# Performance work log

Measured on AMD Instinct MI355X. Metric: run time of the kernel, lower is better.

## Reference

```python
import jax, jax.numpy as jnp
import numpy as np

B, V, D = 8, 2048, 3
CL1_F, CL1_K = 64, 6
CL2_F, CL2_K = 128, 5
F1, F2 = 512, 256


def _uniform(k, shape, fin, fout):
    s = np.sqrt(2.0 / (fin + fout)).astype(np.float32)
    return jax.random.uniform(k, shape, jnp.float32, -s, s)


def setup_inputs() -> dict:
    key = jax.random.key(0)
    ks = jax.random.split(key, 8)
    x = jax.random.normal(ks[0], (B, D, V), jnp.float32)
    # dense stand-in for the scaled graph Laplacian; scaled so spectral radius < 1
    L = jax.random.normal(ks[1], (B, V, V), jnp.float32) * (0.5 / np.sqrt(V))
    L = 0.5 * (L + L.transpose(0, 2, 1))  # symmetric like a real Laplacian
    return {
        "x": x,
        "L": L,
        "cl1_w": _uniform(ks[2], (CL1_F, D * CL1_K), CL1_K, CL1_F),
        "cl1_b": jnp.zeros((CL1_F,), jnp.float32),
        "cl2_w": _uniform(ks[3], (CL2_F, CL2_K * CL1_F), CL2_K * CL1_F, CL2_F),
        "cl2_b": jnp.zeros((CL2_F,), jnp.float32),
        "fc1_w": _uniform(ks[4], (F1, CL2_F), CL2_F, F1),
        "fc1_b": jnp.zeros((F1,), jnp.float32),
        "fc2_w": _uniform(ks[5], (F2, F1), F1, F2),
        "fc2_b": jnp.zeros((F2,), jnp.float32),
    }


def _cheby_conv(x, L, W, b, K):
    # x: [B, V, Fin], L: [B, V, V] -> [B, V, Fout]
    x0 = x
    xs = [x0]
    if K > 1:
        x1 = jnp.einsum('bvu,buf->bvf', L, x0)
        xs.append(x1)
    for _ in range(2, K):
        x2 = 2.0 * jnp.einsum('bvu,buf->bvf', L, x1) - x0
        xs.append(x2)
        x0, x1 = x1, x2
    # torch ordering: feature index = fin * K + k  -> stack K on last axis
    xk = jnp.stack(xs, axis=-1)                 # [B, V, Fin, K]
    xk = xk.reshape(xk.shape[0], xk.shape[1], -1)  # [B, V, Fin*K]
    return xk @ W.T + b


def reference(x, L, cl1_w, cl1_b, cl2_w, cl2_b, fc1_w, fc1_b, fc2_w, fc2_b):
    xp = x.transpose(0, 2, 1)                    # [B, V, D]
    y = jax.nn.relu(_cheby_conv(xp, L, cl1_w, cl1_b, CL1_K))
    y = jax.nn.relu(_cheby_conv(y, L, cl2_w, cl2_b, CL2_K))
    y = jax.nn.relu(y @ fc1_w.T + fc1_b)
    y = jax.nn.relu(y @ fc2_w.T + fc2_b)
    return y                                     # [B, V, F2]
```

## Files before the change

### kernel.cpp

```cpp
#include <hip/hip_runtime.h>

#define B_ 8
#define V_ 2048
#define D_ 3
#define M_ (B_*V_)

typedef __attribute__((ext_vector_type(8))) short short8;
typedef __attribute__((ext_vector_type(4))) float f32x4;

__device__ inline void async_copy16(const void* g, void* lds) {
  __builtin_amdgcn_global_load_lds(
      (const __attribute__((address_space(1))) unsigned int*)g,
      (__attribute__((address_space(3))) unsigned int*)lds, 16, 0, 0);
}

__device__ inline void split_bf16(float v, short& hi, short& lo) {
  unsigned u  = __float_as_uint(v);
  unsigned hb = u & 0xFFFF0000u;
  float d = v - __uint_as_float(hb);
  hi = (short)(hb >> 16);
  lo = (short)(__float_as_uint(d) >> 16);
}

__global__ __launch_bounds__(256) void k_zero(float4* __restrict__ p, int n4) {
  int i = blockIdx.x * 256 + threadIdx.x;
  if (i < n4) p[i] = float4{0.f, 0.f, 0.f, 0.f};
}

__global__ __launch_bounds__(256) void k_split_pad(const float* __restrict__ src,
    short* __restrict__ dh, short* __restrict__ dl, int N, int K, int Kpad) {
  int idx = blockIdx.x * 256 + threadIdx.x;
  if (idx >= N * Kpad) return;
  int n = idx / Kpad, k = idx - n * Kpad;
  float v = (k < K) ? src[(size_t)n*K + k] : 0.f;
  short hi, lo; split_bf16(v, hi, lo);
  dh[idx] = hi; dl[idx] = lo;
}

__global__ __launch_bounds__(256) void k_transpose(const float* __restrict__ x,
    float* __restrict__ x0, short* __restrict__ XKh, short* __restrict__ XKl) {
  int i = blockIdx.x * 256 + threadIdx.x;
  if (i >= B_*V_*D_) return;
  int f = i % D_;
  int v = (i / D_) % V_;
  int b = i / (D_*V_);
  float val = x[((size_t)b*D_ + f)*V_ + v];
  x0[i] = val;
  short hi, lo; split_bf16(val, hi, lo);
  size_t o = ((size_t)b*V_ + v)*64 + f*6;
  XKh[o] = hi; XKl[o] = lo;
}

__global__ __launch_bounds__(256) void k_cheby1(const float* __restrict__ L,
    const float* __restrict__ xc, const float* __restrict__ xp,
    float* __restrict__ xn, short* __restrict__ XKh, short* __restrict__ XKl,
    float alpha, float beta, int kidx) {
  __shared__ float sx[3][V_];
  int b  = blockIdx.x >> 6;
  int r0 = (blockIdx.x & 63) * 32;
  const float* xcb = xc + (size_t)b*V_*D_;
  for (int i = threadIdx.x; i < V_*D_; i += 256) {
    int u = i / 3, f = i - u*3;
    sx[f][u] = xcb[i];
  }
  __syncthreads();
  int w = threadIdx.x >> 6, lane = threadIdx.x & 63;
  const float4* X0 = (const float4*)sx[0];
  const float4* X1 = (const float4*)sx[1];
  const float4* X2 = (const float4*)sx[2];
  for (int pass = 0; pass < 4; pass++) {
    int rA = r0 + pass*8 + w*2;
    int rB = rA + 1;
    const float4* LA = (const float4*)(L + ((size_t)b*V_ + rA)*V_);
    const float4* LB = (const float4*)(L + ((size_t)b*V_ + rB)*V_);
    float a0=0.f,a1=0.f,a2=0.f,b0=0.f,b1=0.f,b2=0.f;
    #pragma unroll
    for (int it = 0; it < 8; it++) {
      int u4 = it*64 + lane;
      float4 la = LA[u4], lb = LB[u4];
      float4 x0 = X0[u4], x1 = X1[u4], x2 = X2[u4];
      a0 = fmaf(la.x,x0.x,fmaf(la.y,x0.y,fmaf(la.z,x0.z,fmaf(la.w,x0.w,a0))));
      a1 = fmaf(la.x,x1.x,fmaf(la.y,x1.y,fmaf(la.z,x1.z,fmaf(la.w,x1.w,a1))));
      a2 = fmaf(la.x,x2.x,fmaf(la.y,x2.y,fmaf(la.z,x2.z,fmaf(la.w,x2.w,a2))));
      b0 = fmaf(lb.x,x0.x,fmaf(lb.y,x0.y,fmaf(lb.z,x0.z,fmaf(lb.w,x0.w,b0))));
      b1 = fmaf(lb.x,x1.x,fmaf(lb.y,x1.y,fmaf(lb.z,x1.z,fmaf(lb.w,x1.w,b1))));
      b2 = fmaf(lb.x,x2.x,fmaf(lb.y,x2.y,fmaf(lb.z,x2.z,fmaf(lb.w,x2.w,b2))));
    }
    #pragma unroll
    for (int off = 32; off > 0; off >>= 1) {
      a0 += __shfl_down(a0, off); a1 += __shfl_down(a1, off);
      a2 += __shfl_down(a2, off); b0 += __shfl_down(b0, off);
      b1 += __shfl_down(b1, off); b2 += __shfl_down(b2, off);
    }
    if (lane == 0) {
      float vA[3] = {alpha*a0, alpha*a1, alpha*a2};
      float vB[3] = {alpha*b0, alpha*b1, alpha*b2};
      size_t baseA = ((size_t)b*V_ + rA)*3;
      size_t baseB = ((size_t)b*V_ + rB)*3;
      if (beta != 0.f) {
        #pragma unroll
        for (int f = 0; f < 3; f++) {
          vA[f] -= beta * xp[baseA + f];
          vB[f] -= beta * xp[baseB + f];
        }
      }
      #pragma unroll
      for (int f = 0; f < 3; f++) {
        xn[baseA + f] = vA[f];
        xn[baseB + f] = vB[f];
        short hi, lo;
        split_bf16(vA[f], hi, lo);
        size_t oA = ((size_t)b*V_ + rA)*64 + f*6 + kidx;
        XKh[oA] = hi; XKl[oA] = lo;
        split_bf16(vB[f], hi, lo);
        size_t oB = ((size_t)b*V_ + rB)*64 + f*6 + kidx;
        XKh[oB] = hi; XKl[oB] = lo;
      }
    }
  }
}

__global__ __launch_bounds__(256) void k_split_t(const float* __restrict__ Z,
    short* __restrict__ Th, short* __restrict__ Tl) {
  __shared__ float t[64][65];
  int b  = blockIdx.x >> 5;
  int r0 = (blockIdx.x & 31) * 64;
  const float* Zb = Z + ((size_t)b*V_ + r0)*64;
  #pragma unroll 4
  for (int i = 0; i < 16; i++) {
    int idx = i*256 + threadIdx.x;
    int r = idx >> 6, n = idx & 63;
    t[r][n] = Zb[(size_t)r*64 + n];
  }
  __syncthreads();
  #pragma unroll 4
  for (int i = 0; i < 16; i++) {
    int idx = i*256 + threadIdx.x;
    int n = idx >> 6, r = idx & 63;
    short hi, lo; split_bf16(t[r][n], hi, lo);
    size_t o = ((size_t)b*64 + n)*V_ + r0 + r;
    Th[o] = hi; Tl[o] = lo;
  }
}

__global__ __launch_bounds__(256) void k_cheby2_mfma(const float* __restrict__ L,
    const short* __restrict__ Zth, const short* __restrict__ Ztl,
    const float* __restrict__ Zp,
    float* __restrict__ Zn, short* __restrict__ ZKh, short* __restrict__ ZKl,
    short* __restrict__ Znth, short* __restrict__ Zntl,
    float alpha, float beta, int kidx) {
  __shared__ float sA[32*64];
  __shared__ short sBh[64*64];
  __shared__ short sBl[64*64];

  int b  = blockIdx.x >> 6;
  int r0 = (blockIdx.x & 63) * 32;
  const float* Lb   = L   + (size_t)b*V_*V_;
  const short* Zthb = Zth + (size_t)b*64*V_;
  const short* Ztlb = Ztl + (size_t)b*64*V_;

  int tid  = threadIdx.x;
  int w    = tid >> 6;
  int lane = tid & 63;
  int lm   = lane & 15;
  int quad = lane >> 4;
  int h     = (w & 1) * 16;
  int cbase = (w >> 1) * 32;

  const f32x4*  sAv  = (const f32x4*)sA;
  const short8* sBhv = (const short8*)sBh;
  const short8* sBlv = (const short8*)sBl;

  f32x4 acc0 = {0.f,0.f,0.f,0.f};
  f32x4 acc1 = {0.f,0.f,0.f,0.f};

  for (int s = 0; s < V_/64; s++) {
    int k0 = s * 64;
    if (s) __syncthreads();
    #pragma unroll
    for (int t = 0; t < 2; t++) {
      int f = t*256 + tid;
      int r = f >> 4, cc = f & 15;
      int c = cc ^ (r & 15);
      async_copy16(Lb + (size_t)(r0 + r)*V_ + k0 + c*4, &sA[f*4]);
    }
    #pragma unroll
    for (int t = 0; t < 2; t++) {
      int f = t*256 + tid;
      int n = f >> 3, cc = f & 7;
      int c = cc ^ (n & 7);
      async_copy16(Zthb + (size_t)n*V_ + k0 + c*8, &sBh[f*8]);
      async_copy16(Ztlb + (size_t)n*V_ + k0 + c*8, &sBl[f*8]);
    }
    __syncthreads();

    #pragma unroll
    for (int ks = 0; ks < 2; ks++) {
      int koff = ks * 32;
      int r = h + lm;
      int c0 = (koff >> 2) + 2*quad;
      f32x4 a0 = sAv[r*16 + (c0 ^ (r & 15))];
      f32x4 a1 = sAv[r*16 + ((c0 + 1) ^ (r & 15))];
      float av[8] = {a0.x, a0.y, a0.z, a0.w, a1.x, a1.y, a1.z, a1.w};
      short8 ah, al;
      #pragma unroll
      for (int j = 0; j < 8; j++) {
        short hi, lo; split_bf16(av[j], hi, lo);
        ah[j] = hi; al[j] = lo;
      }
      int cb = (koff >> 3) + quad;
      {
        int n = cbase + lm;
        short8 bh = sBhv[n*8 + (cb ^ (n & 7))];
        short8 bl = sBlv[n*8 + (cb ^ (n & 7))];
        acc0 = __builtin_amdgcn_mfma_f32_16x16x32_bf16(ah, bh, acc0, 0, 0, 0);
        acc0 = __builtin_amdgcn_mfma_f32_16x16x32_bf16(ah, bl, acc0, 0, 0, 0);
        acc0 = __builtin_amdgcn_mfma_f32_16x16x32_bf16(al, bh, acc0, 0, 0, 0);
      }
      {
        int n = cbase + 16 + lm;
        short8 bh = sBhv[n*8 + (cb ^ (n & 7))];
        short8 bl = sBlv[n*8 + (cb ^ (n & 7))];
        acc1 = __builtin_amdgcn_mfma_f32_16x16x32_bf16(ah, bh, acc1, 0, 0, 0);
        acc1 = __builtin_amdgcn_mfma_f32_16x16x32_bf16(ah, bl, acc1, 0, 0, 0);
        acc1 = __builtin_amdgcn_mfma_f32_16x16x32_bf16(al, bh, acc1, 0, 0, 0);
      }
    }
  }

  #pragma unroll
  for (int ct = 0; ct < 2; ct++) {
    f32x4 a = ct ? acc1 : acc0;
    int n = cbase + ct*16 + lm;
    #pragma unroll
    for (int i = 0; i < 4; i++) {
      int r = r0 + h + quad*4 + i;
      size_t rowb = (size_t)b*V_ + r;
      float v = alpha * a[i];
      if (beta != 0.f) v -= beta * Zp[rowb*64 + n];
      Zn[rowb*64 + n] = v;
      short hi, lo; split_bf16(v, hi, lo);
      size_t ok = rowb*320 + (size_t)n*5 + kidx;
      ZKh[ok] = hi; ZKl[ok] = lo;
      size_t o = ((size_t)b*64 + n)*V_ + r;
      Znth[o] = hi; Zntl[o] = lo;
    }
  }
}

__global__ __launch_bounds__(256) void k_gemm_bf16(
    const short* __restrict__ Ah, const short* __restrict__ Al,
    const short* __restrict__ Wh, const short* __restrict__ Wl,
    const float* __restrict__ bias, int N, int K,
    float* __restrict__ Cf, short* __restrict__ Ch, short* __restrict__ Cl,
    short* __restrict__ Ph, short* __restrict__ Pl,
    int packMul, int packStride) {
  __shared__ short sAh[64*64], sAl[64*64], sWh[64*64], sWl[64*64];
  int bm = blockIdx.x & 255;
  int bn = blockIdx.x >> 8;
  int row0 = bm * 64, col0 = bn * 64;
  int tid = threadIdx.x, w = tid >> 6, lane = tid & 63;
  int lm = lane & 15, quad = lane >> 4;
  int wm = (w & 1) * 32, wn = (w >> 1) * 32;

  const short8* vAh = (const short8*)sAh;
  const short8* vAl = (const short8*)sAl;
  const short8* vWh = (const short8*)sWh;
  const short8* vWl = (const short8*)sWl;

  f32x4 acc[2][2] = {{{0.f,0.f,0.f,0.f},{0.f,0.f,0.f,0.f}},
                     {{0.f,0.f,0.f,0.f},{0.f,0.f,0.f,0.f}}};

  for (int k0 = 0; k0 < K; k0 += 64) {
    if (k0) __syncthreads();
    #pragma unroll
    for (int t = 0; t < 2; t++) {
      int f = t*256 + tid;
      int r = f >> 3, p = f & 7;
      int c = p ^ (r & 7);
      size_t goA = (size_t)(row0 + r)*K + k0 + c*8;
      size_t goW = (size_t)(col0 + r)*K + k0 + c*8;
      async_copy16(Ah + goA, &sAh[f*8]);
      async_copy16(Al + goA, &sAl[f*8]);
      async_copy16(Wh + goW, &sWh[f*8]);
      async_copy16(Wl + goW, &sWl[f*8]);
    }
    __syncthreads();

    #pragma unroll
    for (int ks = 0; ks < 2; ks++) {
      int kc = ks*4 + quad;
      short8 a_h[2], a_l[2], b_h[2], b_l[2];
      #pragma unroll
      for (int i = 0; i < 2; i++) {
        int m = wm + i*16 + lm;
        a_h[i] = vAh[m*8 + (kc ^ (m & 7))];
        a_l[i] = vAl[m*8 + (kc ^ (m & 7))];
      }
      #pragma unroll
      for (int j = 0; j < 2; j++) {
        int n = wn + j*16 + lm;
        b_h[j] = vWh[n*8 + (kc ^ (n & 7))];
        b_l[j] = vWl[n*8 + (kc ^ (n & 7))];
      }
      #pragma unroll
      for (int i = 0; i < 2; i++)
        #pragma unroll
        for (int j = 0; j < 2; j++) {
          acc[i][j] = __builtin_amdgcn_mfma_f32_16x16x32_bf16(a_h[i], b_h[j], acc[i][j], 0, 0, 0);
          acc[i][j] = __builtin_amdgcn_mfma_f32_16x16x32_bf16(a_h[i], b_l[j], acc[i][j], 0, 0, 0);
          acc[i][j] = __builtin_amdgcn_mfma_f32_16x16x32_bf16(a_l[i], b_h[j], acc[i][j], 0, 0, 0);
        }
    }
  }

  #pragma unroll
  for (int i = 0; i < 2; i++)
    #pragma unroll
    for (int j = 0; j < 2; j++) {
      int col = col0 + wn + j*16 + lm;
      float bj = bias[col];
      #pragma unroll
      for (int g = 0; g < 4; g++) {
        int row = row0 + wm + i*16 + quad*4 + g;
        float v = acc[i][j][g] + bj;
        v = v > 0.f ? v : 0.f;
        if (Cf) Cf[(size_t)row*N + col] = v;
        if (Ch) {
          short hi, lo; split_bf16(v, hi, lo);
          Ch[(size_t)row*N + col] = hi;
          Cl[(size_t)row*N + col] = lo;
        }
        if (Ph) {
          short hi, lo; split_bf16(v, hi, lo);
          size_t o = (size_t)row*packStride + (size_t)col*packMul;
          Ph[o] = hi; Pl[o] = lo;
        }
      }
    }
}

extern "C" void kernel_launch(void* const* d_in, const int* in_sizes, int n_in,
                              void* d_out, int out_size, void* d_ws, size_t ws_size,
                              hipStream_t stream) {
  const float* x   = (const float*)d_in[0];
  const float* L   = (const float*)d_in[1];
  const float* w1  = (const float*)d_in[2];
  const float* b1  = (const float*)d_in[3];
  const float* w2  = (const float*)d_in[4];
  const float* b2  = (const float*)d_in[5];
  const float* fw1 = (const float*)d_in[6];
  const float* fb1 = (const float*)d_in[7];
  const float* fw2 = (const float*)d_in[8];
  const float* fb2 = (const float*)d_in[9];
  float* out = (float*)d_out;

  float* p  = (float*)d_ws;
  float* xa = p;  p += (size_t)B_*V_*D_;
  float* xb = p;  p += (size_t)B_*V_*D_;
  float* xc = p;  p += (size_t)B_*V_*D_;
  float* y1 = p;  p += (size_t)M_*64;
  float* zb = p;  p += (size_t)M_*64;
  float* zc = p;  p += (size_t)M_*64;
  short* sp = (short*)p;
  short* ZKh = sp;  sp += (size_t)M_*320;
  short* ZKl = sp;  sp += (size_t)M_*320;
  short* y2h = sp;  sp += (size_t)M_*128;
  short* y2l = sp;  sp += (size_t)M_*128;
  short* h1h = sp;  sp += (size_t)M_*512;
  short* h1l = sp;  sp += (size_t)M_*512;
  short* ZtAh = sp; sp += (size_t)M_*64;
  short* ZtAl = sp; sp += (size_t)M_*64;
  short* ZtBh = sp; sp += (size_t)M_*64;
  short* ZtBl = sp; sp += (size_t)M_*64;
  short* w1h = sp;  sp += 64*64;
  short* w1l = sp;  sp += 64*64;
  short* w2h = sp;  sp += 128*320;
  short* w2l = sp;  sp += 128*320;
  short* fw1h = sp; sp += 512*128;
  short* fw1l = sp; sp += 512*128;
  short* fw2h = sp; sp += 256*512;
  short* fw2l = sp; sp += 256*512;
  short* XKh = h1h;
  short* XKl = h1h + (size_t)M_*64;

  dim3 blk(256);

  k_zero<<<1024, blk, 0, stream>>>((float4*)XKh, (M_*128) / 8);

  k_split_pad<<<(64*64+255)/256,   blk, 0, stream>>>(w1,  w1h,  w1l,  64, 18, 64);
  k_split_pad<<<(128*320+255)/256, blk, 0, stream>>>(w2,  w2h,  w2l,  128, 320, 320);
  k_split_pad<<<(512*128+255)/256, blk, 0, stream>>>(fw1, fw1h, fw1l, 512, 128, 128);
  k_split_pad<<<(256*512+255)/256, blk, 0, stream>>>(fw2, fw2h, fw2l, 256, 512, 512);

  k_transpose<<<(B_*V_*D_ + 255)/256, blk, 0, stream>>>(x, xa, XKh, XKl);

  k_cheby1<<<512, blk, 0, stream>>>(L, xa, xa, xb, XKh, XKl, 1.f, 0.f, 1);
  k_cheby1<<<512, blk, 0, stream>>>(L, xb, xa, xc, XKh, XKl, 2.f, 1.f, 2);
  k_cheby1<<<512, blk, 0, stream>>>(L, xc, xb, xa, XKh, XKl, 2.f, 1.f, 3);
  k_cheby1<<<512, blk, 0, stream>>>(L, xa, xc, xb, XKh, XKl, 2.f, 1.f, 4);
  k_cheby1<<<512, blk, 0, stream>>>(L, xb, xa, xc, XKh, XKl, 2.f, 1.f, 5);

  k_gemm_bf16<<<256, blk, 0, stream>>>(XKh, XKl, w1h, w1l, b1, 64, 64,
                                       y1, nullptr, nullptr, ZKh, ZKl, 5, 320);

  k_split_t<<<256, blk, 0, stream>>>(y1, ZtAh, ZtAl);

  k_cheby2_mfma<<<512, blk, 0, stream>>>(L, ZtAh, ZtAl, y1, zb, ZKh, ZKl,
                                         ZtBh, ZtBl, 1.f, 0.f, 1);
  k_cheby2_mfma<<<512, blk, 0, stream>>>(L, ZtBh, ZtBl, y1, zc, ZKh, ZKl,
                                         ZtAh, ZtAl, 2.f, 1.f, 2);
  k_cheby2_mfma<<<512, blk, 0, stream>>>(L, ZtAh, ZtAl, zb, y1, ZKh, ZKl,
                                         ZtBh, ZtBl, 2.f, 1.f, 3);
  k_cheby2_mfma<<<512, blk, 0, stream>>>(L, ZtBh, ZtBl, zc, zb, ZKh, ZKl,
                                         ZtAh, ZtAl, 2.f, 1.f, 4);

  k_gemm_bf16<<<512, blk, 0, stream>>>(ZKh, ZKl, w2h, w2l, b2, 128, 320,
                                       nullptr, y2h, y2l, nullptr, nullptr, 0, 0);
  k_gemm_bf16<<<2048, blk, 0, stream>>>(y2h, y2l, fw1h, fw1l, fb1, 512, 128,
                                        nullptr, h1h, h1l, nullptr, nullptr, 0, 0);
  k_gemm_bf16<<<1024, blk, 0, stream>>>(h1h, h1l, fw2h, fw2l, fb2, 256, 512,
                                        out, nullptr, nullptr, nullptr, nullptr, 0, 0);
}
```

Measured before the change: 594.7 us.

## Merge stage launches into cooperative persistent kernels with grid syncs

Replaces many small launches with a few: a combined prep kernel (zeroing, transpose, weight splitting), cooperative kernels that run all Chebyshev steps of each layer with grid.sync between steps, and a cooperative kernel chaining the three dense GEMMs. The layer-1 GEMM epilogue now also writes the transposed bf16 split, which removes the separate transpose kernel. The aim is to cut launch gaps and inter-kernel idle time. In exchange it relies on 512 blocks being co-resident and adds grid-wide barrier cost, and the FC GEMMs with 2048 or 1024 tiles now loop over a fixed 512-block grid.

```diff
diff --git a/kernel.cpp b/kernel.cpp
--- a/kernel.cpp
+++ b/kernel.cpp
@@ -1,4 +1,7 @@
 #include <hip/hip_runtime.h>
+#include <hip/hip_cooperative_groups.h>
+
+namespace cg = cooperative_groups;
 
 #define B_ 8
 #define V_ 2048
@@ -22,243 +25,139 @@
   lo = (short)(__float_as_uint(d) >> 16);
 }
 
-__global__ __launch_bounds__(256) void k_zero(float4* __restrict__ p, int n4) {
+__global__ __launch_bounds__(256) void k_prep(
+    const float* __restrict__ x,
+    const float* __restrict__ w1, const float* __restrict__ w2,
+    const float* __restrict__ fw1, const float* __restrict__ fw2,
+    float* __restrict__ xa,
+    short* __restrict__ XKh, short* __restrict__ XKl,
+    short* __restrict__ w1h, short* __restrict__ w1l,
+    short* __restrict__ w2h, short* __restrict__ w2l,
+    short* __restrict__ fw1h, short* __restrict__ fw1l,
+    short* __restrict__ fw2h, short* __restrict__ fw2l) {
   int i = blockIdx.x * 256 + threadIdx.x;
-  if (i < n4) p[i] = float4{0.f, 0.f, 0.f, 0.f};
-}
-
-__global__ __launch_bounds__(256) void k_split_pad(const float* __restrict__ src,
-    short* __restrict__ dh, short* __restrict__ dl, int N, int K, int Kpad) {
-  int idx = blockIdx.x * 256 + threadIdx.x;
-  if (idx >= N * Kpad) return;
-  int n = idx / Kpad, k = idx - n * Kpad;
-  float v = (k < K) ? src[(size_t)n*K + k] : 0.f;
-  short hi, lo; split_bf16(v, hi, lo);
-  dh[idx] = hi; dl[idx] = lo;
-}
-
-__global__ __launch_bounds__(256) void k_transpose(const float* __restrict__ x,
-    float* __restrict__ x0, short* __restrict__ XKh, short* __restrict__ XKl) {
-  int i = blockIdx.x * 256 + threadIdx.x;
-  if (i >= B_*V_*D_) return;
-  int f = i % D_;
-  int v = (i / D_) % V_;
-  int b = i / (D_*V_);
-  float val = x[((size_t)b*D_ + f)*V_ + v];
-  x0[i] = val;
-  short hi, lo; split_bf16(val, hi, lo);
-  size_t o = ((size_t)b*V_ + v)*64 + f*6;
-  XKh[o] = hi; XKl[o] = lo;
-}
-
-__global__ __launch_bounds__(256) void k_cheby1(const float* __restrict__ L,
-    const float* __restrict__ xc, const float* __restrict__ xp,
-    float* __restrict__ xn, short* __restrict__ XKh, short* __restrict__ XKl,
-    float alpha, float beta, int kidx) {
+  short hi, lo;
+  if (i < M_*64) {
+    int r = i >> 6, s = i & 63;
+    float val = 0.f;
+    if (s == 0 || s == 6 || s == 12) {
+      int f = s / 6;
+      int b = r >> 11, v = r & (V_-1);
+      val = x[((size_t)b*D_ + f)*V_ + v];
+      xa[(size_t)r*3 + f] = val;
+    }
+    split_bf16(val, hi, lo);
+    XKh[i] = hi; XKl[i] = lo;
+    return;
+  }
+  i -= M_*64;
+  if (i < 4096) {
+    int n = i >> 6, k = i & 63;
+    float v = (k < 18) ? w1[n*18 + k] : 0.f;
+    split_bf16(v, hi, lo); w1h[i] = hi; w1l[i] = lo; return;
+  }
+  i -= 4096;
+  if (i < 40960) { split_bf16(w2[i],  hi, lo); w2h[i]=hi;  w2l[i]=lo;  return; }
+  i -= 40960;
+  if (i < 65536) { split_bf16(fw1[i], hi, lo); fw1h[i]=hi; fw1l[i]=lo; return; }
+  i -= 65536;
+  if (i < 131072){ split_bf16(fw2[i], hi, lo); fw2h[i]=hi; fw2l[i]=lo; return; }
+}
+
+__global__ __launch_bounds__(256, 2) void k_cheby1_all(
+    const float* __restrict__ L, float* __restrict__ xa,
+    float* __restrict__ xb, float* __restrict__ xc,
+    short* __restrict__ XKh, short* __restrict__ XKl) {
+  cg::grid_group grid = cg::this_grid();
   __shared__ float sx[3][V_];
+
+  const float* srcs[5]  = {xa, xb, xc, xa, xb};
+  const float* prevs[5] = {xa, xa, xb, xc, xa};
+  float*       dsts[5]  = {xb, xc, xa, xb, xc};
+
   int b  = blockIdx.x >> 6;
   int r0 = (blockIdx.x & 63) * 32;
-  const float* xcb = xc + (size_t)b*V_*D_;
-  for (int i = threadIdx.x; i < V_*D_; i += 256) {
-    int u = i / 3, f = i - u*3;
-    sx[f][u] = xcb[i];
-  }
-  __syncthreads();
   int w = threadIdx.x >> 6, lane = threadIdx.x & 63;
-  const float4* X0 = (const float4*)sx[0];
-  const float4* X1 = (const float4*)sx[1];
-  const float4* X2 = (const float4*)sx[2];
-  for (int pass = 0; pass < 4; pass++) {
-    int rA = r0 + pass*8 + w*2;
-    int rB = rA + 1;
-    const float4* LA = (const float4*)(L + ((size_t)b*V_ + rA)*V_);
-    const float4* LB = (const float4*)(L + ((size_t)b*V_ + rB)*V_);
-    float a0=0.f,a1=0.f,a2=0.f,b0=0.f,b1=0.f,b2=0.f;
-    #pragma unroll
-    for (int it = 0; it < 8; it++) {
-      int u4 = it*64 + lane;
-      float4 la = LA[u4], lb = LB[u4];
-      float4 x0 = X0[u4], x1 = X1[u4], x2 = X2[u4];
-      a0 = fmaf(la.x,x0.x,fmaf(la.y,x0.y,fmaf(la.z,x0.z,fmaf(la.w,x0.w,a0))));
-      a1 = fmaf(la.x,x1.x,fmaf(la.y,x1.y,fmaf(la.z,x1.z,fmaf(la.w,x1.w,a1))));
-      a2 = fmaf(la.x,x2.x,fmaf(la.y,x2.y,fmaf(la.z,x2.z,fmaf(la.w,x2.w,a2))));
-      b0 = fmaf(lb.x,x0.x,fmaf(lb.y,x0.y,fmaf(lb.z,x0.z,fmaf(lb.w,x0.w,b0))));
-      b1 = fmaf(lb.x,x1.x,fmaf(lb.y,x1.y,fmaf(lb.z,x1.z,fmaf(lb.w,x1.w,b1))));
-      b2 = fmaf(lb.x,x2.x,fmaf(lb.y,x2.y,fmaf(lb.z,x2.z,fmaf(lb.w,x2.w,b2))));
-    }
-    #pragma unroll
-    for (int off = 32; off > 0; off >>= 1) {
-      a0 += __shfl_down(a0, off); a1 += __shfl_down(a1, off);
-      a2 += __shfl_down(a2, off); b0 += __shfl_down(b0, off);
-      b1 += __shfl_down(b1, off); b2 += __shfl_down(b2, off);
-    }
-    if (lane == 0) {
-      float vA[3] = {alpha*a0, alpha*a1, alpha*a2};
-      float vB[3] = {alpha*b0, alpha*b1, alpha*b2};
-      size_t baseA = ((size_t)b*V_ + rA)*3;
-      size_t baseB = ((size_t)b*V_ + rB)*3;
-      if (beta != 0.f) {
+
+  for (int step = 0; step < 5; step++) {
+    float alpha = (step == 0) ? 1.f : 2.f;
+    bool  haveP = (step != 0);
+    const float* xcb = srcs[step] + (size_t)b*V_*D_;
+    const float* xp  = prevs[step];
+    float* xn = dsts[step];
+    int kidx = step + 1;
+
+    for (int i = threadIdx.x; i < V_*D_; i += 256) {
+      int u = i / 3, f = i - u*3;
+      sx[f][u] = xcb[i];
+    }
+    __syncthreads();
+
+    const float4* X0 = (const float4*)sx[0];
+    const float4* X1 = (const float4*)sx[1];
+    const float4* X2 = (const float4*)sx[2];
+    for (int pass = 0; pass < 4; pass++) {
+      int rA = r0 + pass*8 + w*2;
+      int rB = rA + 1;
+      const float4* LA = (const float4*)(L + ((size_t)b*V_ + rA)*V_);
+      const float4* LB = (const float4*)(L + ((size_t)b*V_ + rB)*V_);
+      float a0=0.f,a1=0.f,a2=0.f,b0=0.f,b1=0.f,b2=0.f;
+      #pragma unroll
+      for (int it = 0; it < 8; it++) {
+        int u4 = it*64 + lane;
+        float4 la = LA[u4], lb = LB[u4];
+        float4 x0 = X0[u4], x1 = X1[u4], x2 = X2[u4];
+        a0 = fmaf(la.x,x0.x,fmaf(la.y,x0.y,fmaf(la.z,x0.z,fmaf(la.w,x0.w,a0))));
+        a1 = fmaf(la.x,x1.x,fmaf(la.y,x1.y,fmaf(la.z,x1.z,fmaf(la.w,x1.w,a1))));
+        a2 = fmaf(la.x,x2.x,fmaf(la.y,x2.y,fmaf(la.z,x2.z,fmaf(la.w,x2.w,a2))));
+        b0 = fmaf(lb.x,x0.x,fmaf(lb.y,x0.y,fmaf(lb.z,x0.z,fmaf(lb.w,x0.w,b0))));
+        b1 = fmaf(lb.x,x1.x,fmaf(lb.y,x1.y,fmaf(lb.z,x1.z,fmaf(lb.w,x1.w,b1))));
+        b2 = fmaf(lb.x,x2.x,fmaf(lb.y,x2.y,fmaf(lb.z,x2.z,fmaf(lb.w,x2.w,b2))));
+      }
+      #pragma unroll
+      for (int off = 32; off > 0; off >>= 1) {
+        a0 += __shfl_down(a0, off); a1 += __shfl_down(a1, off);
+        a2 += __shfl_down(a2, off); b0 += __shfl_down(b0, off);
+        b1 += __shfl_down(b1, off); b2 += __shfl_down(b2, off);
+      }
+      if (lane == 0) {
+        float vA[3] = {alpha*a0, alpha*a1, alpha*a2};
+        float vB[3] = {alpha*b0, alpha*b1, alpha*b2};
+        size_t baseA = ((size_t)b*V_ + rA)*3;
+        size_t baseB = ((size_t)b*V_ + rB)*3;
+        if (haveP) {
+          #pragma unroll
+          for (int f = 0; f < 3; f++) {
+            vA[f] -= xp[baseA + f];
+            vB[f] -= xp[baseB + f];
+          }
+        }
         #pragma unroll
         for (int f = 0; f < 3; f++) {
-          vA[f] -= beta * xp[baseA + f];
-          vB[f] -= beta * xp[baseB + f];
-        }
-      }
-      #pragma unroll
-      for (int f = 0; f < 3; f++) {
-        xn[baseA + f] = vA[f];
-        xn[baseB + f] = vB[f];
-        short hi, lo;
-        split_bf16(vA[f], hi, lo);
-        size_t oA = ((size_t)b*V_ + rA)*64 + f*6 + kidx;
-        XKh[oA] = hi; XKl[oA] = lo;
-        split_bf16(vB[f], hi, lo);
-        size_t oB = ((size_t)b*V_ + rB)*64 + f*6 + kidx;
-        XKh[oB] = hi; XKl[oB] = lo;
-      }
-    }
-  }
-}
-
-__global__ __launch_bounds__(256) void k_split_t(const float* __restrict__ Z,
-    short* __restrict__ Th, short* __restrict__ Tl) {
-  __shared__ float t[64][65];
-  int b  = blockIdx.x >> 5;
-  int r0 = (blockIdx.x & 31) * 64;
-  const float* Zb = Z + ((size_t)b*V_ + r0)*64;
-  #pragma unroll 4
-  for (int i = 0; i < 16; i++) {
-    int idx = i*256 + threadIdx.x;
-    int r = idx >> 6, n = idx & 63;
-    t[r][n] = Zb[(size_t)r*64 + n];
-  }
-  __syncthreads();
-  #pragma unroll 4
-  for (int i = 0; i < 16; i++) {
-    int idx = i*256 + threadIdx.x;
-    int n = idx >> 6, r = idx & 63;
-    short hi, lo; split_bf16(t[r][n], hi, lo);
-    size_t o = ((size_t)b*64 + n)*V_ + r0 + r;
-    Th[o] = hi; Tl[o] = lo;
-  }
-}
-
-__global__ __launch_bounds__(256) void k_cheby2_mfma(const float* __restrict__ L,
-    const short* __restrict__ Zth, const short* __restrict__ Ztl,
-    const float* __restrict__ Zp,
-    float* __restrict__ Zn, short* __restrict__ ZKh, short* __restrict__ ZKl,
-    short* __restrict__ Znth, short* __restrict__ Zntl,
-    float alpha, float beta, int kidx) {
-  __shared__ float sA[32*64];
-  __shared__ short sBh[64*64];
-  __shared__ short sBl[64*64];
-
-  int b  = blockIdx.x >> 6;
-  int r0 = (blockIdx.x & 63) * 32;
-  const float* Lb   = L   + (size_t)b*V_*V_;
-  const short* Zthb = Zth + (size_t)b*64*V_;
-  const short* Ztlb = Ztl + (size_t)b*64*V_;
-
-  int tid  = threadIdx.x;
-  int w    = tid >> 6;
-  int lane = tid & 63;
-  int lm   = lane & 15;
-  int quad = lane >> 4;
-  int h     = (w & 1) * 16;
-  int cbase = (w >> 1) * 32;
-
-  const f32x4*  sAv  = (const f32x4*)sA;
-  const short8* sBhv = (const short8*)sBh;
-  const short8* sBlv = (const short8*)sBl;
-
-  f32x4 acc0 = {0.f,0.f,0.f,0.f};
-  f32x4 acc1 = {0.f,0.f,0.f,0.f};
-
-  for (int s = 0; s < V_/64; s++) {
-    int k0 = s * 64;
-    if (s) __syncthreads();
-    #pragma unroll
-    for (int t = 0; t < 2; t++) {
-      int f = t*256 + tid;
-      int r = f >> 4, cc = f & 15;
-      int c = cc ^ (r & 15);
-      async_copy16(Lb + (size_t)(r0 + r)*V_ + k0 + c*4, &sA[f*4]);
-    }
-    #pragma unroll
-    for (int t = 0; t < 2; t++) {
-      int f = t*256 + tid;
-      int n = f >> 3, cc = f & 7;
-      int c = cc ^ (n & 7);
-      async_copy16(Zthb + (size_t)n*V_ + k0 + c*8, &sBh[f*8]);
-      async_copy16(Ztlb + (size_t)n*V_ + k0 + c*8, &sBl[f*8]);
-    }
-    __syncthreads();
-
-    #pragma unroll
-    for (int ks = 0; ks < 2; ks++) {
-      int koff = ks * 32;
-      int r = h + lm;
-      int c0 = (koff >> 2) + 2*quad;
-      f32x4 a0 = sAv[r*16 + (c0 ^ (r & 15))];
-      f32x4 a1 = sAv[r*16 + ((c0 + 1) ^ (r & 15))];
-      float av[8] = {a0.x, a0.y, a0.z, a0.w, a1.x, a1.y, a1.z, a1.w};
-      short8 ah, al;
-      #pragma unroll
-      for (int j = 0; j < 8; j++) {
-        short hi, lo; split_bf16(av[j], hi, lo);
-        ah[j] = hi; al[j] = lo;
-      }
-      int cb = (koff >> 3) + quad;
-      {
-        int n = cbase + lm;
-        short8 bh = sBhv[n*8 + (cb ^ (n & 7))];
-        short8 bl = sBlv[n*8 + (cb ^ (n & 7))];
-        acc0 = __builtin_amdgcn_mfma_f32_16x16x32_bf16(ah, bh, acc0, 0, 0, 0);
-        acc0 = __builtin_amdgcn_mfma_f32_16x16x32_bf16(ah, bl, acc0, 0, 0, 0);
-        acc0 = __builtin_amdgcn_mfma_f32_16x16x32_bf16(al, bh, acc0, 0, 0, 0);
-      }
-      {
-        int n = cbase + 16 + lm;
-        short8 bh = sBhv[n*8 + (cb ^ (n & 7))];
-        short8 bl = sBlv[n*8 + (cb ^ (n & 7))];
-        acc1 = __builtin_amdgcn_mfma_f32_16x16x32_bf16(ah, bh, acc1, 0, 0, 0);
-        acc1 = __builtin_amdgcn_mfma_f32_16x16x32_bf16(ah, bl, acc1, 0, 0, 0);
-        acc1 = __builtin_amdgcn_mfma_f32_16x16x32_bf16(al, bh, acc1, 0, 0, 0);
-      }
-    }
-  }
-
-  #pragma unroll
-  for (int ct = 0; ct < 2; ct++) {
-    f32x4 a = ct ? acc1 : acc0;
-    int n = cbase + ct*16 + lm;
-    #pragma unroll
-    for (int i = 0; i < 4; i++) {
-      int r = r0 + h + quad*4 + i;
-      size_t rowb = (size_t)b*V_ + r;
-      float v = alpha * a[i];
-      if (beta != 0.f) v -= beta * Zp[rowb*64 + n];
-      Zn[rowb*64 + n] = v;
-      short hi, lo; split_bf16(v, hi, lo);
-      size_t ok = rowb*320 + (size_t)n*5 + kidx;
-      ZKh[ok] = hi; ZKl[ok] = lo;
-      size_t o = ((size_t)b*64 + n)*V_ + r;
-      Znth[o] = hi; Zntl[o] = lo;
-    }
-  }
-}
-
-__global__ __launch_bounds__(256) void k_gemm_bf16(
+          xn[baseA + f] = vA[f];
+          xn[baseB + f] = vB[f];
+          short hi, lo;
+          split_bf16(vA[f], hi, lo);
+          size_t oA = ((size_t)b*V_ + rA)*64 + f*6 + kidx;
+          XKh[oA] = hi; XKl[oA] = lo;
+          split_bf16(vB[f], hi, lo);
+          size_t oB = ((size_t)b*V_ + rB)*64 + f*6 + kidx;
+          XKh[oB] = hi; XKl[oB] = lo;
+        }
+      }
+    }
+    grid.sync();
+  }
+}
+
+__device__ __forceinline__ void gemm_tile(
     const short* __restrict__ Ah, const short* __restrict__ Al,
     const short* __restrict__ Wh, const short* __restrict__ Wl,
-    const float* __restrict__ bias, int N, int K,
+    const float* __restrict__ bias, int N, int K, int row0, int col0,
+    short* sAh, short* sAl, short* sWh, short* sWl,
     float* __restrict__ Cf, short* __restrict__ Ch, short* __restrict__ Cl,
-    short* __restrict__ Ph, short* __restrict__ Pl,
-    int packMul, int packStride) {
-  __shared__ short sAh[64*64], sAl[64*64], sWh[64*64], sWl[64*64];
-  int bm = blockIdx.x & 255;
-  int bn = blockIdx.x >> 8;
-  int row0 = bm * 64, col0 = bn * 64;
+    short* __restrict__ Ph, short* __restrict__ Pl, int packMul, int packStride,
+    short* __restrict__ Th, short* __restrict__ Tl) {
   int tid = threadIdx.x, w = tid >> 6, lane = tid & 63;
   int lm = lane & 15, quad = lane >> 4;
   int wm = (w & 1) * 32, wn = (w >> 1) * 32;
@@ -272,7 +171,7 @@
                      {{0.f,0.f,0.f,0.f},{0.f,0.f,0.f,0.f}}};
 
   for (int k0 = 0; k0 < K; k0 += 64) {
-    if (k0) __syncthreads();
+    __syncthreads();
     #pragma unroll
     for (int t = 0; t < 2; t++) {
       int f = t*256 + tid;
@@ -326,18 +225,187 @@
         float v = acc[i][j][g] + bj;
         v = v > 0.f ? v : 0.f;
         if (Cf) Cf[(size_t)row*N + col] = v;
+        short hi, lo;
+        if (Ch || Ph || Th) split_bf16(v, hi, lo);
         if (Ch) {
-          short hi, lo; split_bf16(v, hi, lo);
           Ch[(size_t)row*N + col] = hi;
           Cl[(size_t)row*N + col] = lo;
         }
         if (Ph) {
-          short hi, lo; split_bf16(v, hi, lo);
           size_t o = (size_t)row*packStride + (size_t)col*packMul;
           Ph[o] = hi; Pl[o] = lo;
         }
-      }
-    }
+        if (Th) {
+          int bb = row >> 11, vv = row & (V_-1);
+          size_t o = ((size_t)bb*64 + col)*V_ + vv;
+          Th[o] = hi; Tl[o] = lo;
+        }
+      }
+    }
+}
+
+__global__ __launch_bounds__(256) void k_gemm_y1(
+    const short* __restrict__ XKh, const short* __restrict__ XKl,
+    const short* __restrict__ w1h, const short* __restrict__ w1l,
+    const float* __restrict__ b1, float* __restrict__ y1,
+    short* __restrict__ ZKh, short* __restrict__ ZKl,
+    short* __restrict__ Th, short* __restrict__ Tl) {
+  __shared__ short sAh[64*64], sAl[64*64], sWh[64*64], sWl[64*64];
+  gemm_tile(XKh, XKl, w1h, w1l, b1, 64, 64, blockIdx.x*64, 0,
+            sAh, sAl, sWh, sWl,
+            y1, nullptr, nullptr, ZKh, ZKl, 5, 320, Th, Tl);
+}
+
+__global__ __launch_bounds__(256, 2) void k_cheby2_all(const float* __restrict__ L,
+    short* __restrict__ ZtAh, short* __restrict__ ZtAl,
+    short* __restrict__ ZtBh, short* __restrict__ ZtBl,
+    float* __restrict__ y1, float* __restrict__ zb, float* __restrict__ zc,
+    short* __restrict__ ZKh, short* __restrict__ ZKl) {
+  cg::grid_group grid = cg::this_grid();
+  __shared__ float sA[32*64];
+  __shared__ short sBh[64*64];
+  __shared__ short sBl[64*64];
+
+  int b  = blockIdx.x >> 6;
+  int r0 = (blockIdx.x & 63) * 32;
+  const float* Lb = L + (size_t)b*V_*V_;
+
+  int tid = threadIdx.x, w = tid >> 6, lane = tid & 63;
+  int lm = lane & 15, quad = lane >> 4;
+  int h = (w & 1) * 16, cbase = (w >> 1) * 32;
+
+  const f32x4*  sAv  = (const f32x4*)sA;
+  const short8* sBhv = (const short8*)sBh;
+  const short8* sBlv = (const short8*)sBl;
+
+  const short* Bh[4] = {ZtAh, ZtBh, ZtAh, ZtBh};
+  const short* Bl[4] = {ZtAl, ZtBl, ZtAl, ZtBl};
+  short* Thh[4] = {ZtBh, ZtAh, ZtBh, ZtAh};
+  short* Tll[4] = {ZtBl, ZtAl, ZtBl, ZtAl};
+  const float* Zp[4] = {nullptr, y1, zb, zc};
+  float* Zd[4] = {zb, zc, y1, zb};
+
+  for (int step = 0; step < 4; step++) {
+    float alpha = (step == 0) ? 1.f : 2.f;
+    const short* Zthb = Bh[step] + (size_t)b*64*V_;
+    const short* Ztlb = Bl[step] + (size_t)b*64*V_;
+    f32x4 acc0 = {0.f,0.f,0.f,0.f};
+    f32x4 acc1 = {0.f,0.f,0.f,0.f};
+
+    for (int s = 0; s < V_/64; s++) {
+      int k0 = s * 64;
+      if (s) __syncthreads();
+      #pragma unroll
+      for (int t = 0; t < 2; t++) {
+        int f = t*256 + tid;
+        int r = f >> 4, cc = f & 15;
+        int c = cc ^ (r & 15);
+        async_copy16(Lb + (size_t)(r0 + r)*V_ + k0 + c*4, &sA[f*4]);
+      }
+      #pragma unroll
+      for (int t = 0; t < 2; t++) {
+        int f = t*256 + tid;
+        int n = f >> 3, cc = f & 7;
+        int c = cc ^ (n & 7);
+        async_copy16(Zthb + (size_t)n*V_ + k0 + c*8, &sBh[f*8]);
+        async_copy16(Ztlb + (size_t)n*V_ + k0 + c*8, &sBl[f*8]);
+      }
+      __syncthreads();
+
+      #pragma unroll
+      for (int ks = 0; ks < 2; ks++) {
+        int koff = ks * 32;
+        int r = h + lm;
+        int c0 = (koff >> 2) + 2*quad;
+        f32x4 a0 = sAv[r*16 + (c0 ^ (r & 15))];
+        f32x4 a1 = sAv[r*16 + ((c0 + 1) ^ (r & 15))];
+        float av[8] = {a0.x, a0.y, a0.z, a0.w, a1.x, a1.y, a1.z, a1.w};
+        short8 ah, al;
+        #pragma unroll
+        for (int j = 0; j < 8; j++) {
+          short hi, lo; split_bf16(av[j], hi, lo);
+          ah[j] = hi; al[j] = lo;
+        }
+        int cb = (koff >> 3) + quad;
+        {
+          int n = cbase + lm;
+          short8 bh = sBhv[n*8 + (cb ^ (n & 7))];
+          short8 bl = sBlv[n*8 + (cb ^ (n & 7))];
+          acc0 = __builtin_amdgcn_mfma_f32_16x16x32_bf16(ah, bh, acc0, 0, 0, 0);
+          acc0 = __builtin_amdgcn_mfma_f32_16x16x32_bf16(ah, bl, acc0, 0, 0, 0);
+          acc0 = __builtin_amdgcn_mfma_f32_16x16x32_bf16(al, bh, acc0, 0, 0, 0);
+        }
+        {
+          int n = cbase + 16 + lm;
+          short8 bh = sBhv[n*8 + (cb ^ (n & 7))];
+          short8 bl = sBlv[n*8 + (cb ^ (n & 7))];
+          acc1 = __builtin_amdgcn_mfma_f32_16x16x32_bf16(ah, bh, acc1, 0, 0, 0);
+          acc1 = __builtin_amdgcn_mfma_f32_16x16x32_bf16(ah, bl, acc1, 0, 0, 0);
+          acc1 = __builtin_amdgcn_mfma_f32_16x16x32_bf16(al, bh, acc1, 0, 0, 0);
+        }
+      }
+    }
+
+    const float* zp = Zp[step];
+    float* zn = Zd[step];
+    short* Tho = Thh[step];
+    short* Tlo = Tll[step];
+    #pragma unroll
+    for (int ct = 0; ct < 2; ct++) {
+      f32x4 a = ct ? acc1 : acc0;
+      int n = cbase + ct*16 + lm;
+      #pragma unroll
+      for (int i = 0; i < 4; i++) {
+        int r = r0 + h + quad*4 + i;
+        size_t rowb = (size_t)b*V_ + r;
+        float v = alpha * a[i];
+        if (zp) v -= zp[rowb*64 + n];
+        zn[rowb*64 + n] = v;
+        short hi, lo; split_bf16(v, hi, lo);
+        size_t ok = rowb*320 + (size_t)n*5 + (step + 1);
+        ZKh[ok] = hi; ZKl[ok] = lo;
+        size_t o = ((size_t)b*64 + n)*V_ + r;
+        Tho[o] = hi; Tlo[o] = lo;
+      }
+    }
+    grid.sync();
+  }
+}
+
+__global__ __launch_bounds__(256, 2) void k_fc_chain(
+    const short* __restrict__ ZKh, const short* __restrict__ ZKl,
+    const short* __restrict__ w2h, const short* __restrict__ w2l,
+    const float* __restrict__ b2,
+    short* __restrict__ y2h, short* __restrict__ y2l,
+    const short* __restrict__ fw1h, const short* __restrict__ fw1l,
+    const float* __restrict__ fb1,
+    short* __restrict__ h1h, short* __restrict__ h1l,
+    const short* __restrict__ fw2h, const short* __restrict__ fw2l,
+    const float* __restrict__ fb2,
+    float* __restrict__ out) {
+  cg::grid_group grid = cg::this_grid();
+  __shared__ short sAh[64*64], sAl[64*64], sWh[64*64], sWl[64*64];
+
+  for (int t = blockIdx.x; t < 512; t += 512) {
+    int bm = t & 255, bn = t >> 8;
+    gemm_tile(ZKh, ZKl, w2h, w2l, b2, 128, 320, bm*64, bn*64,
+              sAh, sAl, sWh, sWl,
+              nullptr, y2h, y2l, nullptr, nullptr, 0, 0, nullptr, nullptr);
+  }
+  grid.sync();
+  for (int t = blockIdx.x; t < 2048; t += 512) {
+    int bm = t & 255, bn = t >> 8;
+    gemm_tile(y2h, y2l, fw1h, fw1l, fb1, 512, 128, bm*64, bn*64,
+              sAh, sAl, sWh, sWl,
+              nullptr, h1h, h1l, nullptr, nullptr, 0, 0, nullptr, nullptr);
+  }
+  grid.sync();
+  for (int t = blockIdx.x; t < 1024; t += 512) {
+    int bm = t & 255, bn = t >> 8;
+    gemm_tile(h1h, h1l, fw2h, fw2l, fb2, 256, 512, bm*64, bn*64,
+              sAh, sAl, sWh, sWl,
+              out, nullptr, nullptr, nullptr, nullptr, 0, 0, nullptr, nullptr);
+  }
 }
 
 extern "C" void kernel_launch(void* const* d_in, const int* in_sizes, int n_in,
@@ -384,41 +452,35 @@
   short* XKh = h1h;
   short* XKl = h1h + (size_t)M_*64;
 
-  dim3 blk(256);
-
-  k_zero<<<1024, blk, 0, stream>>>((float4*)XKh, (M_*128) / 8);
-
-  k_split_pad<<<(64*64+255)/256,   blk, 0, stream>>>(w1,  w1h,  w1l,  64, 18, 64);
-  k_split_pad<<<(128*320+255)/256, blk, 0, stream>>>(w2,  w2h,  w2l,  128, 320, 320);
-  k_split_pad<<<(512*128+255)/256, blk, 0, stream>>>(fw1, fw1h, fw1l, 512, 128, 128);
-  k_split_pad<<<(256*512+255)/256, blk, 0, stream>>>(fw2, fw2h, fw2l, 256, 512, 512);
-
-  k_transpose<<<(B_*V_*D_ + 255)/256, blk, 0, stream>>>(x, xa, XKh, XKl);
-
-  k_cheby1<<<512, blk, 0, stream>>>(L, xa, xa, xb, XKh, XKl, 1.f, 0.f, 1);
-  k_cheby1<<<512, blk, 0, stream>>>(L, xb, xa, xc, XKh, XKl, 2.f, 1.f, 2);
-  k_cheby1<<<512, blk, 0, stream>>>(L, xc, xb, xa, XKh, XKl, 2.f, 1.f, 3);
-  k_cheby1<<<512, blk, 0, stream>>>(L, xa, xc, xb, XKh, XKl, 2.f, 1.f, 4);
-  k_cheby1<<<512, blk, 0, stream>>>(L, xb, xa, xc, XKh, XKl, 2.f, 1.f, 5);
-
-  k_gemm_bf16<<<256, blk, 0, stream>>>(XKh, XKl, w1h, w1l, b1, 64, 64,
-                                       y1, nullptr, nullptr, ZKh, ZKl, 5, 320);
-
-  k_split_t<<<256, blk, 0, stream>>>(y1, ZtAh, ZtAl);
-
-  k_cheby2_mfma<<<512, blk, 0, stream>>>(L, ZtAh, ZtAl, y1, zb, ZKh, ZKl,
-                                         ZtBh, ZtBl, 1.f, 0.f, 1);
-  k_cheby2_mfma<<<512, blk, 0, stream>>>(L, ZtBh, ZtBl, y1, zc, ZKh, ZKl,
-                                         ZtAh, ZtAl, 2.f, 1.f, 2);
-  k_cheby2_mfma<<<512, blk, 0, stream>>>(L, ZtAh, ZtAl, zb, y1, ZKh, ZKl,
-                                         ZtBh, ZtBl, 2.f, 1.f, 3);
-  k_cheby2_mfma<<<512, blk, 0, stream>>>(L, ZtBh, ZtBl, zc, zb, ZKh, ZKl,
-                                         ZtAh, ZtAl, 2.f, 1.f, 4);
-
-  k_gemm_bf16<<<512, blk, 0, stream>>>(ZKh, ZKl, w2h, w2l, b2, 128, 320,
-                                       nullptr, y2h, y2l, nullptr, nullptr, 0, 0);
-  k_gemm_bf16<<<2048, blk, 0, stream>>>(y2h, y2l, fw1h, fw1l, fb1, 512, 128,
-                                        nullptr, h1h, h1l, nullptr, nullptr, 0, 0);
-  k_gemm_bf16<<<1024, blk, 0, stream>>>(h1h, h1l, fw2h, fw2l, fb2, 256, 512,
-                                        out, nullptr, nullptr, nullptr, nullptr, 0, 0);
-}
+  k_prep<<<5040, 256, 0, stream>>>(x, w1, w2, fw1, fw2, xa,
+                                   XKh, XKl, w1h, w1l, w2h, w2l,
+                                   fw1h, fw1l, fw2h, fw2l);
+
+  {
+    void* a[] = {(void*)&L, (void*)&xa, (void*)&xb, (void*)&xc,
+                 (void*)&XKh, (void*)&XKl};
+    hipLaunchCooperativeKernel((void*)k_cheby1_all, dim3(512), dim3(256),
+                               a, 0, stream);
+  }
+
+  k_gemm_y1<<<256, 256, 0, stream>>>(XKh, XKl, w1h, w1l, b1,
+                                     y1, ZKh, ZKl, ZtAh, ZtAl);
+
+  {
+    void* a[] = {(void*)&L, (void*)&ZtAh, (void*)&ZtAl, (void*)&ZtBh,
+                 (void*)&ZtBl, (void*)&y1, (void*)&zb, (void*)&zc,
+                 (void*)&ZKh, (void*)&ZKl};
+    hipLaunchCooperativeKernel((void*)k_cheby2_all, dim3(512), dim3(256),
+                               a, 0, stream);
+  }
+
+  {
+    void* a[] = {(void*)&ZKh, (void*)&ZKl, (void*)&w2h, (void*)&w2l,
+                 (void*)&b2, (void*)&y2h, (void*)&y2l,
+                 (void*)&fw1h, (void*)&fw1l, (void*)&fb1,
+                 (void*)&h1h, (void*)&h1l,
+                 (void*)&fw2h, (void*)&fw2l, (void*)&fb2, (void*)&out};
+    hipLaunchCooperativeKernel((void*)k_fc_chain, dim3(512), dim3(256),
+                               a, 0, stream);
+  }
+}
```

Result: slower. 1.353 ms (+127.5%).
